# Optimization experiments

Measured on AMD Instinct MI355X. Metric: run time of the kernel, lower is better.

## Reference

```python
import jax, jax.numpy as jnp
import numpy as np

C, CP, H, D, N, B = 128, 16, 8, 16, 2048, 1
INF = 1e8


def _ln(x, w=None, b=None, eps=1e-5):
    mu = jnp.mean(x, axis=-1, keepdims=True)
    var = jnp.var(x, axis=-1, keepdims=True)
    y = (x - mu) * jax.lax.rsqrt(var + eps)
    if w is not None:
        y = y * w
    if b is not None:
        y = y + b
    return y


def _ada_ln(a, s, sln_w, gw, gb, skw):
    # AdaLN: non-affine LN on a, weight-only LN on s, sigmoid gate + skip from s
    a = _ln(a)
    s = _ln(s, sln_w)
    return jax.nn.sigmoid(s @ gw + gb) * a + s @ skw


def _betas(n, n_keys=128, inf=INF):
    # centers at 16 + 32k; query row i belongs to window i//32, keys within +/- n_keys//2 of center
    i = jnp.arange(n)
    c = 16 + 32 * (i // 32)
    j = jnp.arange(n)
    ok = (j[None, :] >= (c - n_keys // 2)[:, None]) & (j[None, :] < (c + n_keys // 2)[:, None])
    return jnp.where(ok, 0.0, -inf).astype(jnp.float32)


def _forward(atom_single, atom_proj, atom_pair, mask,
             a_sln_w, a_gate_w, a_gate_b, a_skip_w,
             wq, bq, wk, wv, wg, bg, wo, bo,
             lnz_w, lnz_b, wz, wog, bog,
             t_sln_w, t_gate_w, t_gate_b, t_skip_w,
             w_sw, w_hid, w_out, t_wog, t_bog):
    bs, n, _ = atom_single.shape
    betas = _betas(n)
    # ---- AttentionPairBias (input_gating=True, residual handled outside) ----
    a = _ada_ln(atom_single, atom_proj, a_sln_w, a_gate_w, a_gate_b, a_skip_w)
    q = (a @ wq + bq).reshape(bs, n, H, D)
    k = (a @ wk).reshape(bs, n, H, D)
    v = (a @ wv).reshape(bs, n, H, D)
    pair_bias = _ln(atom_pair, lnz_w, lnz_b) @ wz            # (bs, n, n, H)
    pair_bias = jnp.transpose(pair_bias, (0, 3, 1, 2)) + betas  # (bs, H, n, n)
    mask_bias = (INF * (mask - 1.0))[:, None, None, :]          # (bs, 1, 1, n)
    logits = jnp.einsum('bqhd,bkhd->bhqk', q, k) / np.float32(np.sqrt(D))
    logits = logits + pair_bias + mask_bias
    probs = jax.nn.softmax(logits, axis=-1)
    o = jnp.einsum('bhqk,bkhd->bqhd', probs, v)
    g = jax.nn.sigmoid(a @ wg + bg).reshape(bs, n, H, D)
    o = (o * g).reshape(bs, n, H * D) @ wo + bo
    o = jax.nn.sigmoid(atom_proj @ wog + bog) * o             # conditioned output gate
    atom_single = atom_single + o
    # ---- ConditionedTransitionBlock (SwiGLU, n=2) ----
    t = _ada_ln(atom_single, atom_proj, t_sln_w, t_gate_w, t_gate_b, t_skip_w)
    hidden = jax.nn.silu(t @ w_sw) * (t @ w_hid)              # (bs, n, 2C)
    t_out = jax.nn.sigmoid(atom_proj @ t_wog + t_bog) * (hidden @ w_out)
    return atom_single + t_out


def setup_inputs() -> dict:
    key = jax.random.key(0)
    ks = iter(jax.random.split(key, 40))
    rn = lambda shape, s=1.0: jax.random.normal(next(ks), shape, jnp.float32) * s
    p = 0.05
    return {
        "atom_single": rn((B, N, C)),
        "atom_proj": rn((B, N, C)),
        "atom_pair": rn((B, N, N, CP)),
        "mask": jnp.ones((B, N), jnp.float32),
        "a_sln_w": jnp.ones((C,), jnp.float32), "a_gate_w": rn((C, C), p), "a_gate_b": jnp.zeros((C,), jnp.float32), "a_skip_w": rn((C, C), p),
        "wq": rn((C, C), p), "bq": jnp.zeros((C,), jnp.float32),
        "wk": rn((C, C), p), "wv": rn((C, C), p),
        "wg": rn((C, C), p), "bg": jnp.ones((C,), jnp.float32),
        "wo": rn((C, C), p), "bo": jnp.zeros((C,), jnp.float32),
        "lnz_w": jnp.ones((CP,), jnp.float32), "lnz_b": jnp.zeros((CP,), jnp.float32), "wz": rn((CP, H), p),
        "wog": rn((C, C), p), "bog": jnp.full((C,), -2.0, jnp.float32),
        "t_sln_w": jnp.ones((C,), jnp.float32), "t_gate_w": rn((C, C), p), "t_gate_b": jnp.zeros((C,), jnp.float32), "t_skip_w": rn((C, C), p),
        "w_sw": rn((C, 2 * C), p), "w_hid": rn((C, 2 * C), p), "w_out": rn((2 * C, C), p),
        "t_wog": rn((C, C), p), "t_bog": jnp.full((C,), -2.0, jnp.float32),
    }


def reference(atom_single, atom_proj, atom_pair, mask,
              a_sln_w, a_gate_w, a_gate_b, a_skip_w,
              wq, bq, wk, wv, wg, bg, wo, bo,
              lnz_w, lnz_b, wz, wog, bog,
              t_sln_w, t_gate_w, t_gate_b, t_skip_w,
              w_sw, w_hid, w_out, t_wog, t_bog):
    out = _forward(atom_single, atom_proj, atom_pair, mask,
                   a_sln_w, a_gate_w, a_gate_b, a_skip_w,
                   wq, bq, wk, wv, wg, bg, wo, bo,
                   lnz_w, lnz_b, wz, wog, bog,
                   t_sln_w, t_gate_w, t_gate_b, t_skip_w,
                   w_sw, w_hid, w_out, t_wog, t_bog)
    return (out, atom_proj, atom_pair)
```

## Files before the change

kernel.cpp:

```cpp
#include <hip/hip_runtime.h>
#include <math.h>

#define NN 2048
#define CC 128
#define HH 8
#define DD 16
#define NKEY 128
#define INFV 1e8f
#define NPR ((long)NN * CC / 4)
#define NCPTOT (NPR + (long)NN * NN * 4)
#define SLOT 2176
#define ANP 36
#define ASLOT 1152

__device__ __forceinline__ float sigm(float x) { return 1.f / (1.f + expf(-x)); }

struct Args {
  const float *atom_single, *atom_proj, *atom_pair, *mask;
  const float *a_sln_w, *a_gate_w, *a_gate_b, *a_skip_w;
  const float *wq, *bq, *wk, *wv, *wg, *bg, *wo, *bo;
  const float *lnz_w, *lnz_b, *wz, *wog, *bog;
  const float *t_sln_w, *t_gate_w, *t_gate_b, *t_skip_w;
  const float *w_sw, *w_hid, *w_out, *t_wog, *t_bog;
  float *out;
  float *s_ln_a, *s_ln_t, *ln_as, *a_mat, *qm, *km, *vm, *gm, *ogm,
        *single2, *t_mat, *hidden, *bias;
  long cut[9];
};

__device__ __forceinline__ void copy_span(const Args& a, int s, long rb, long nb, int tid) {
  long c0 = a.cut[s], c1 = a.cut[s + 1];
  const float4* proj4 = (const float4*)a.atom_proj;
  const float4* pair4 = (const float4*)a.atom_pair;
  float4* dst = (float4*)(a.out + (long)NN * CC);
  long stride = nb * 256;
  long i = c0 + rb * 256 + tid;
  for (; i + 3 * stride < c1; i += 4 * stride) {
    long i1 = i + stride, i2 = i + 2 * stride, i3 = i + 3 * stride;
    float4 x0 = (i  < NPR) ? proj4[i]  : pair4[i  - NPR];
    float4 x1 = (i1 < NPR) ? proj4[i1] : pair4[i1 - NPR];
    float4 x2 = (i2 < NPR) ? proj4[i2] : pair4[i2 - NPR];
    float4 x3 = (i3 < NPR) ? proj4[i3] : pair4[i3 - NPR];
    dst[i] = x0; dst[i1] = x1; dst[i2] = x2; dst[i3] = x3;
  }
  for (; i < c1; i += stride) dst[i] = (i < NPR) ? proj4[i] : pair4[i - NPR];
}

__device__ __forceinline__ void gsingle_pf(float* sm, int tid,
    const float* __restrict__ A1, const float* __restrict__ B1, int lda1, int ldb1, int K1,
    int r0, int c0, float acc1[4][4]) {
  float* buf0 = sm;
  float* buf1 = sm + 2 * SLOT;
  int tr = (tid >> 4) * 4, tc = (tid & 15) * 4;
  int ar = tid >> 5, ak = tid & 31;
  int bk = tid >> 6, bc = tid & 63;
  float pA[2][8], pB[2][8];
  auto LD = [&](int kb, int s) {
#pragma unroll
    for (int j = 0; j < 8; ++j) {
      pA[s][j] = A1[(long)(r0 + ar + 8 * j) * lda1 + kb + ak];
      pB[s][j] = B1[(long)(kb + bk + 4 * j) * ldb1 + c0 + bc];
    }
  };
  auto WR = [&](float* buf, int s) {
    float* B1s_ = buf + SLOT;
#pragma unroll
    for (int j = 0; j < 8; ++j) {
      buf[ak * 68 + ar + 8 * j] = pA[s][j];
      B1s_[(bk + 4 * j) * 68 + bc] = pB[s][j];
    }
  };
  auto CMP = [&](float* cur) {
    float* As_ = cur;
    float* B1s_ = cur + SLOT;
#pragma unroll 4
    for (int k = 0; k < 32; ++k) {
      float4 a1 = *(const float4*)&As_[k * 68 + tr];
      float4 b1 = *(const float4*)&B1s_[k * 68 + tc];
      float a1v[4] = {a1.x, a1.y, a1.z, a1.w};
      float b1v[4] = {b1.x, b1.y, b1.z, b1.w};
#pragma unroll
      for (int i = 0; i < 4; ++i)
#pragma unroll
        for (int j = 0; j < 4; ++j) acc1[i][j] = fmaf(a1v[i], b1v[j], acc1[i][j]);
    }
  };
  int nk = K1 / 32;
  LD(0, 0);
  if (nk > 1) LD(32, 1);
  WR(buf0, 0);
  __syncthreads();
  for (int kt = 0; kt < nk; kt += 2) {
    if (kt + 2 < nk) LD((kt + 2) * 32, 0);
    if (kt + 1 < nk) WR(buf1, 1);
    CMP(buf0);
    __syncthreads();
    if (kt + 1 >= nk) break;
    if (kt + 3 < nk) LD((kt + 3) * 32, 1);
    if (kt + 2 < nk) WR(buf0, 0);
    CMP(buf1);
    __syncthreads();
  }
}

template <bool SHA>
__device__ __forceinline__ void gdual32(float* sm, int tid,
    const float* __restrict__ A1, const float* __restrict__ B1, int lda1, int ldb1, int K1,
    const float* __restrict__ A2, const float* __restrict__ B2, int lda2, int ldb2, int K2,
    int r0, int c0, float acc1[2][4], float acc2[2][4]) {
  const int offB1 = ASLOT;
  const int offA2 = ASLOT + SLOT;
  const int offB2 = SHA ? (ASLOT + SLOT) : (2 * ASLOT + SLOT);
  const int bufsz = SHA ? (ASLOT + 2 * SLOT) : (2 * ASLOT + 2 * SLOT);
  float* buf0 = sm;
  float* buf1 = sm + bufsz;
  int tr2 = (tid >> 4) * 2, tc4 = (tid & 15) * 4;
  int ar = tid & 31, ak4 = (tid >> 5) * 4;
  int bk = tid >> 6, bc = tid & 63;
  float4 vA1[2], vA2[2];
  float pB1[2][8], pB2[2][8];

  auto LD = [&](int kb, int s, bool twof) {
    vA1[s] = *(const float4*)&A1[(long)(r0 + ar) * lda1 + kb + ak4];
#pragma unroll
    for (int j = 0; j < 8; ++j)
      pB1[s][j] = B1[(long)(kb + bk + 4 * j) * ldb1 + c0 + bc];
    if (twof) {
      if constexpr (!SHA) vA2[s] = *(const float4*)&A2[(long)(r0 + ar) * lda2 + kb + ak4];
#pragma unroll
      for (int j = 0; j < 8; ++j)
        pB2[s][j] = B2[(long)(kb + bk + 4 * j) * ldb2 + c0 + bc];
    }
  };
  auto WR = [&](float* buf, int s, bool twof) {
    float* As_ = buf;
    float* B1s_ = buf + offB1;
    As_[(ak4 + 0) * ANP + ar] = vA1[s].x;
    As_[(ak4 + 1) * ANP + ar] = vA1[s].y;
    As_[(ak4 + 2) * ANP + ar] = vA1[s].z;
    As_[(ak4 + 3) * ANP + ar] = vA1[s].w;
#pragma unroll
    for (int j = 0; j < 8; ++j) B1s_[(bk + 4 * j) * 68 + bc] = pB1[s][j];
    if (twof) {
      float* B2s_ = buf + offB2;
      if constexpr (!SHA) {
        float* A2s_ = buf + offA2;
        A2s_[(ak4 + 0) * ANP + ar] = vA2[s].x;
        A2s_[(ak4 + 1) * ANP + ar] = vA2[s].y;
        A2s_[(ak4 + 2) * ANP + ar] = vA2[s].z;
        A2s_[(ak4 + 3) * ANP + ar] = vA2[s].w;
      }
#pragma unroll
      for (int j = 0; j < 8; ++j) B2s_[(bk + 4 * j) * 68 + bc] = pB2[s][j];
    }
  };
  auto CMP = [&](float* cur, bool twoc) {
    float* As_ = cur;
    float* B1s_ = cur + offB1;
    float* A2s_ = cur + offA2;
    float* B2s_ = cur + offB2;
    if (twoc) {
#pragma unroll 4
      for (int k = 0; k < 32; ++k) {
        float2 a1 = *(const float2*)&As_[k * ANP + tr2];
        float4 b1 = *(const float4*)&B1s_[k * 68 + tc4];
        float4 b2 = *(const float4*)&B2s_[k * 68 + tc4];
        float2 a2;
        if constexpr (SHA) a2 = a1; else a2 = *(const float2*)&A2s_[k * ANP + tr2];
        float a1v[2] = {a1.x, a1.y};
        float a2v[2] = {a2.x, a2.y};
        float b1v[4] = {b1.x, b1.y, b1.z, b1.w};
        float b2v[4] = {b2.x, b2.y, b2.z, b2.w};
#pragma unroll
        for (int i = 0; i < 2; ++i)
#pragma unroll
          for (int j = 0; j < 4; ++j) {
            acc1[i][j] = fmaf(a1v[i], b1v[j], acc1[i][j]);
            acc2[i][j] = fmaf(a2v[i], b2v[j], acc2[i][j]);
          }
      }
    } else {
#pragma unroll 4
      for (int k = 0; k < 32; ++k) {
        float2 a1 = *(const float2*)&As_[k * ANP + tr2];
        float4 b1 = *(const float4*)&B1s_[k * 68 + tc4];
        float a1v[2] = {a1.x, a1.y};
        float b1v[4] = {b1.x, b1.y, b1.z, b1.w};
#pragma unroll
        for (int i = 0; i < 2; ++i)
#pragma unroll
          for (int j = 0; j < 4; ++j) acc1[i][j] = fmaf(a1v[i], b1v[j], acc1[i][j]);
      }
    }
  };

  int nk = K1 / 32;
  LD(0, 0, 0 < K2);
  if (nk > 1) LD(32, 1, 32 < K2);
  WR(buf0, 0, 0 < K2);
  __syncthreads();
  for (int kt = 0; kt < nk; kt += 2) {
    if (kt + 2 < nk) LD((kt + 2) * 32, 0, (kt + 2) * 32 < K2);
    if (kt + 1 < nk) WR(buf1, 1, (kt + 1) * 32 < K2);
    CMP(buf0, kt * 32 < K2);
    __syncthreads();
    if (kt + 1 >= nk) break;
    if (kt + 3 < nk) LD((kt + 3) * 32, 1, (kt + 3) * 32 < K2);
    if (kt + 2 < nk) WR(buf0, 0, (kt + 2) * 32 < K2);
    CMP(buf1, (kt + 1) * 32 < K2);
    __syncthreads();
  }
}

__device__ __forceinline__ void bias_stage(const Args& a, long lo, long hi,
                                           int bid, int nb, int tid, float* sm) {
  float* swz = sm;
  float* swn = sm + 128;
  float* sbn = sm + 144;
  if (tid < 128) swz[tid] = a.wz[tid];
  else if (tid < 144) swn[tid - 128] = a.lnz_w[tid - 128];
  else if (tid < 160) sbn[tid - 144] = a.lnz_b[tid - 144];
  __syncthreads();
  for (long e = lo + bid * 256 + tid; e < hi; e += (long)nb * 256) {
    int q = (int)(e >> 7), kk = (int)(e & 127);
    int k = (q >> 5) * 32 - 48 + kk;
    float o[HH];
    if (k >= 0 && k < NN) {
      const float4* p = (const float4*)(a.atom_pair + ((long)q * NN + k) * 16);
      float4 x0 = p[0], x1 = p[1], x2 = p[2], x3 = p[3];
      float x[16] = {x0.x, x0.y, x0.z, x0.w, x1.x, x1.y, x1.z, x1.w,
                     x2.x, x2.y, x2.z, x2.w, x3.x, x3.y, x3.z, x3.w};
      float s = 0.f, ss = 0.f;
#pragma unroll
      for (int c = 0; c < 16; ++c) { s += x[c]; ss += x[c] * x[c]; }
      float mu = s * (1.f / 16.f);
      float r = rsqrtf(ss * (1.f / 16.f) - mu * mu + 1e-5f);
#pragma unroll
      for (int h = 0; h < HH; ++h) o[h] = 0.f;
#pragma unroll
      for (int c = 0; c < 16; ++c) {
        float y = (x[c] - mu) * r * swn[c] + sbn[c];
#pragma unroll
        for (int h = 0; h < HH; ++h) o[h] = fmaf(y, swz[c * HH + h], o[h]);
      }
      float mb = INFV * (a.mask[k] - 1.f);
#pragma unroll
      for (int h = 0; h < HH; ++h) o[h] += mb;
    } else {
#pragma unroll
      for (int h = 0; h < HH; ++h) o[h] = -INFV;
    }
#pragma unroll
    for (int h = 0; h < HH; ++h) a.bias[(long)h * NN * NKEY + e] = o[h];
  }
}

__device__ __forceinline__ void ln1_stage(const Args& a, int lb, int tid) {
  int base = lb * 64;
  int lane = tid & 63;
  for (int r = base + (tid >> 6); r < base + 64; r += 4) {
    {
      float2 v = *(const float2*)(a.atom_single + (long)r * CC + lane * 2);
      float s = v.x + v.y, ss = v.x * v.x + v.y * v.y;
#pragma unroll
      for (int m = 1; m < 64; m <<= 1) { s += __shfl_xor(s, m); ss += __shfl_xor(ss, m); }
      float mu = s * (1.f / CC);
      float rr = rsqrtf(ss * (1.f / CC) - mu * mu + 1e-5f);
      *(float2*)(a.ln_as + (long)r * CC + lane * 2) =
          make_float2((v.x - mu) * rr, (v.y - mu) * rr);
    }
    {
      float2 v = *(const float2*)(a.atom_proj + (long)r * CC + lane * 2);
      float s = v.x + v.y, ss = v.x * v.x + v.y * v.y;
#pragma unroll
      for (int m = 1; m < 64; m <<= 1) { s += __shfl_xor(s, m); ss += __shfl_xor(ss, m); }
      float mu = s * (1.f / CC);
      float rr = rsqrtf(ss * (1.f / CC) - mu * mu + 1e-5f);
      float y0 = (v.x - mu) * rr, y1 = (v.y - mu) * rr;
      float2 wa = *(const float2*)(a.a_sln_w + lane * 2);
      float2 wt = *(const float2*)(a.t_sln_w + lane * 2);
      *(float2*)(a.s_ln_a + (long)r * CC + lane * 2) = make_float2(y0 * wa.x, y1 * wa.y);
      *(float2*)(a.s_ln_t + (long)r * CC + lane * 2) = make_float2(y0 * wt.x, y1 * wt.y);
    }
  }
}

template <bool INLN>
__device__ __forceinline__ void adaln32_stage(const Args& a, const float* A, const float* gw,
                                              const float* gb, const float* skw,
                                              const float* lnm_or_src, float* outp,
                                              int bid, int tid, float* sm, float* sst) {
  int r0 = (bid & 63) * 32, c0 = (bid >> 6) * 64;
  if constexpr (INLN) {
    int row = tid >> 3, cg = (tid & 7) * 16;
    const float* src = lnm_or_src + (long)(r0 + row) * CC + cg;
    float s = 0.f, ss = 0.f;
#pragma unroll
    for (int j = 0; j < 4; ++j) {
      float4 v = *(const float4*)(src + j * 4);
      s += v.x + v.y + v.z + v.w;
      ss += v.x * v.x + v.y * v.y + v.z * v.z + v.w * v.w;
    }
#pragma unroll
    for (int m = 1; m < 8; m <<= 1) { s += __shfl_xor(s, m); ss += __shfl_xor(ss, m); }
    if ((tid & 7) == 0) {
      float mu = s * (1.f / CC);
      sst[2 * row] = mu;
      sst[2 * row + 1] = rsqrtf(ss * (1.f / CC) - mu * mu + 1e-5f);
    }
  }
  float acc1[2][4] = {{0}}, acc2[2][4] = {{0}};
  gdual32<true>(sm, tid, A, gw, 128, 128, 128, A, skw, 128, 128, 128, r0, c0, acc1, acc2);
  int tr2 = (tid >> 4) * 2, tc4 = (tid & 15) * 4;
#pragma unroll
  for (int i = 0; i < 2; ++i) {
    long r = r0 + tr2 + i;
    float lv[4];
    if constexpr (INLN) {
      float mu = sst[2 * (tr2 + i)], rr = sst[2 * (tr2 + i) + 1];
      float4 sv = *(const float4*)(lnm_or_src + r * CC + c0 + tc4);
      lv[0] = (sv.x - mu) * rr; lv[1] = (sv.y - mu) * rr;
      lv[2] = (sv.z - mu) * rr; lv[3] = (sv.w - mu) * rr;
    } else {
      float4 lm = *(const float4*)(lnm_or_src + r * CC + c0 + tc4);
      lv[0] = lm.x; lv[1] = lm.y; lv[2] = lm.z; lv[3] = lm.w;
    }
    float o[4];
#pragma unroll
    for (int j = 0; j < 4; ++j)
      o[j] = sigm(acc1[i][j] + gb[c0 + tc4 + j]) * lv[j] + acc2[i][j];
    *(float4*)(outp + r * CC + c0 + tc4) = make_float4(o[0], o[1], o[2], o[3]);
  }
}

__device__ __forceinline__ void gemm4_stage(const Args& a, int bid, int tid, float* sm) {
  int r0 = (bid & 31) * 64;
  int cg4 = (bid >> 5) * 64;
  int mat = cg4 >> 7;
  int c0 = cg4 & 127;
  const float* B = (mat == 0) ? a.wq : (mat == 1) ? a.wk : (mat == 2) ? a.wv : a.wg;
  float acc[4][4] = {{0}};
  gsingle_pf(sm, tid, a.a_mat, B, 128, 128, 128, r0, c0, acc);
  float* outp = (mat == 0) ? a.qm : (mat == 1) ? a.km : (mat == 2) ? a.vm : a.gm;
  int tr = (tid >> 4) * 4, tc = (tid & 15) * 4;
#pragma unroll
  for (int i = 0; i < 4; ++i) {
    long r = r0 + tr + i;
    float o[4];
#pragma unroll
    for (int j = 0; j < 4; ++j) {
      float x = acc[i][j];
      if (mat == 0) x += a.bq[c0 + tc + j];
      if (mat == 3) x = sigm(x + a.bg[c0 + tc + j]);
      o[j] = x;
    }
    *(float4*)(outp + r * CC + c0 + tc) = make_float4(o[0], o[1], o[2], o[3]);
  }
}

__device__ __forceinline__ void attn_unit(const Args& a, int u, int tid, float* sm) {
  int w = u & 63, h = u >> 6;
  int q0 = w * 32, k0 = w * 32 - 48;
  float* Qs = sm;
  float* Ks = sm + 544;
  float* Vs = sm + 3104;
  float* Ps = sm + 5664;
  for (int i = tid; i < 32 * 16; i += 256) {
    int qi = i >> 4, d = i & 15;
    Qs[qi * 17 + d] = a.qm[(long)(q0 + qi) * CC + h * DD + d];
  }
  for (int i = tid; i < 128 * 16; i += 256) {
    int kk = i >> 4, d = i & 15;
    int k = k0 + kk;
    bool ok = (k >= 0 && k < NN);
    Ks[kk * 20 + d] = ok ? a.km[(long)k * CC + h * DD + d] : 0.f;
    Vs[kk * 20 + d] = ok ? a.vm[(long)k * CC + h * DD + d] : 0.f;
  }
  __syncthreads();
  int qi = tid >> 3, kg = tid & 7;
  const float* brow = a.bias + (long)h * NN * NKEY + (long)(q0 + qi) * NKEY;
  float qreg[16];
#pragma unroll
  for (int d = 0; d < 16; ++d) qreg[d] = Qs[qi * 17 + d];
  float l[16];
#pragma unroll
  for (int j = 0; j < 16; ++j) {
    int kk = kg + 8 * j;
    const float4* kr = (const float4*)&Ks[kk * 20];
    float4 k0v = kr[0], k1v = kr[1], k2v = kr[2], k3v = kr[3];
    float acc = 0.f;
    acc = fmaf(qreg[0], k0v.x, acc);  acc = fmaf(qreg[1], k0v.y, acc);
    acc = fmaf(qreg[2], k0v.z, acc);  acc = fmaf(qreg[3], k0v.w, acc);
    acc = fmaf(qreg[4], k1v.x, acc);  acc = fmaf(qreg[5], k1v.y, acc);
    acc = fmaf(qreg[6], k1v.z, acc);  acc = fmaf(qreg[7], k1v.w, acc);
    acc = fmaf(qreg[8], k2v.x, acc);  acc = fmaf(qreg[9], k2v.y, acc);
    acc = fmaf(qreg[10], k2v.z, acc); acc = fmaf(qreg[11], k2v.w, acc);
    acc = fmaf(qreg[12], k3v.x, acc); acc = fmaf(qreg[13], k3v.y, acc);
    acc = fmaf(qreg[14], k3v.z, acc); acc = fmaf(qreg[15], k3v.w, acc);
    l[j] = acc * 0.25f + brow[kk];
  }
  float m = l[0];
#pragma unroll
  for (int j = 1; j < 16; ++j) m = fmaxf(m, l[j]);
#pragma unroll
  for (int mm = 1; mm < 8; mm <<= 1) m = fmaxf(m, __shfl_xor(m, mm));
  float sum = 0.f;
#pragma unroll
  for (int j = 0; j < 16; ++j) { l[j] = expf(l[j] - m); sum += l[j]; }
#pragma unroll
  for (int mm = 1; mm < 8; mm <<= 1) sum += __shfl_xor(sum, mm);
  float inv = 1.f / sum;
#pragma unroll
  for (int j = 0; j < 16; ++j) Ps[qi * 132 + kg + 8 * j] = l[j] * inv;
  __syncthreads();
  int d0 = tid & 7;
  float o0 = 0.f, o1 = 0.f;
#pragma unroll 8
  for (int kk = 0; kk < 128; ++kk) {
    float p = Ps[qi * 132 + kk];
    o0 = fmaf(p, Vs[kk * 20 + d0], o0);
    o1 = fmaf(p, Vs[kk * 20 + d0 + 8], o1);
  }
  long base = (long)(q0 + qi) * CC + h * DD;
  a.ogm[base + d0] = o0 * a.gm[base + d0];
  a.ogm[base + d0 + 8] = o1 * a.gm[base + d0 + 8];
}

__device__ __forceinline__ void out1_32(const Args& a, int bid, int tid, float* sm) {
  int r0 = (bid & 63) * 32, c0 = (bid >> 6) * 64;
  float accX[2][4] = {{0}}, accW[2][4] = {{0}};
  gdual32<false>(sm, tid, a.ogm, a.wo, 128, 128, 128, a.atom_proj, a.wog, 128, 128, 128,
                 r0, c0, accX, accW);
  int tr2 = (tid >> 4) * 2, tc4 = (tid & 15) * 4;
#pragma unroll
  for (int i = 0; i < 2; ++i) {
    long r = r0 + tr2 + i;
    float4 sv = *(const float4*)(a.atom_single + r * CC + c0 + tc4);
    float s[4] = {sv.x, sv.y, sv.z, sv.w};
    float o[4];
#pragma unroll
    for (int j = 0; j < 4; ++j) {
      int c = c0 + tc4 + j;
      o[j] = s[j] + sigm(accW[i][j] + a.bog[c]) * (accX[i][j] + a.bo[c]);
    }
    *(float4*)(a.single2 + r * CC + c0 + tc4) = make_float4(o[0], o[1], o[2], o[3]);
  }
}

__device__ __forceinline__ void swiglu_32(const Args& a, int bid, int tid, float* sm) {
  int r0 = (bid & 63) * 32, c0 = (bid >> 6) * 64;
  float acc1[2][4] = {{0}}, acc2[2][4] = {{0}};
  gdual32<true>(sm, tid, a.t_mat, a.w_sw, 128, 256, 128, a.t_mat, a.w_hid, 128, 256, 128,
                r0, c0, acc1, acc2);
  int tr2 = (tid >> 4) * 2, tc4 = (tid & 15) * 4;
#pragma unroll
  for (int i = 0; i < 2; ++i) {
    long r = r0 + tr2 + i;
    float o[4];
#pragma unroll
    for (int j = 0; j < 4; ++j) {
      float x = acc1[i][j];
      o[j] = x * sigm(x) * acc2[i][j];
    }
    *(float4*)(a.hidden + r * 256 + c0 + tc4) = make_float4(o[0], o[1], o[2], o[3]);
  }
}

__device__ __forceinline__ void out2_32(const Args& a, int bid, int tid, float* sm) {
  int r0 = (bid & 63) * 32, c0 = (bid >> 6) * 64;
  float accX[2][4] = {{0}}, accW[2][4] = {{0}};
  gdual32<false>(sm, tid, a.hidden, a.w_out, 256, 128, 256, a.atom_proj, a.t_wog, 128, 128, 128,
                 r0, c0, accX, accW);
  int tr2 = (tid >> 4) * 2, tc4 = (tid & 15) * 4;
#pragma unroll
  for (int i = 0; i < 2; ++i) {
    long r = r0 + tr2 + i;
    float4 sv = *(const float4*)(a.single2 + r * CC + c0 + tc4);
    float s[4] = {sv.x, sv.y, sv.z, sv.w};
    float o[4];
#pragma unroll
    for (int j = 0; j < 4; ++j) {
      int c = c0 + tc4 + j;
      o[j] = s[j] + sigm(accW[i][j] + a.t_bog[c]) * accX[i][j];
    }
    *(float4*)(a.out + r * CC + c0 + tc4) = make_float4(o[0], o[1], o[2], o[3]);
  }
}

#define BIAS_TOT ((long)NN * NKEY)
#define BIAS_1 (BIAS_TOT / 3)
#define BIAS_2 (2 * BIAS_TOT / 3)

__global__ __launch_bounds__(256) void k_head(Args a) {
  __shared__ __align__(16) float sm[160];
  int bid = blockIdx.x, tid = threadIdx.x;
  if (bid < 96) bias_stage(a, 0, BIAS_1, bid, 96, tid, sm);
  else if (bid < 128) ln1_stage(a, bid - 96, tid);
  else copy_span(a, 0, bid - 128, gridDim.x - 128, tid);
}

__global__ __launch_bounds__(256) void k_adaln_a(Args a) {
  __shared__ __align__(16) float sm[2 * (ASLOT + 2 * SLOT) + 64];
  int bid = blockIdx.x, tid = threadIdx.x;
  if (bid < 128)
    adaln32_stage<false>(a, a.s_ln_a, a.a_gate_w, a.a_gate_b, a.a_skip_w, a.ln_as, a.a_mat,
                         bid, tid, sm, nullptr);
  else if (bid < 224) bias_stage(a, BIAS_1, BIAS_2, bid - 128, 96, tid, sm);
  else copy_span(a, 1, bid - 224, gridDim.x - 224, tid);
}

__global__ __launch_bounds__(256) void k_qkvg(Args a) {
  __shared__ __align__(16) float sm[2 * 2 * SLOT];
  int bid = blockIdx.x, tid = threadIdx.x;
  if (bid < 256) gemm4_stage(a, bid, tid, sm);
  else if (bid < 352) bias_stage(a, BIAS_2, BIAS_TOT, bid - 256, 96, tid, sm);
  else copy_span(a, 2, bid - 352, gridDim.x - 352, tid);
}

__global__ __launch_bounds__(256) void k_attn(Args a) {
  __shared__ __align__(16) float sm[9888];
  int bid = blockIdx.x, tid = threadIdx.x;
  if (bid < 512) attn_unit(a, bid, tid, sm);
  else copy_span(a, 3, bid - 512, gridDim.x - 512, tid);
}

__global__ __launch_bounds__(256) void k_out1(Args a) {
  __shared__ __align__(16) float sm[2 * (2 * ASLOT + 2 * SLOT)];
  int bid = blockIdx.x, tid = threadIdx.x;
  if (bid < 128) out1_32(a, bid, tid, sm);
  else copy_span(a, 4, bid - 128, gridDim.x - 128, tid);
}

__global__ __launch_bounds__(256) void k_adaln_t(Args a) {
  __shared__ __align__(16) float sm[2 * (ASLOT + 2 * SLOT) + 64];
  int bid = blockIdx.x, tid = threadIdx.x;
  if (bid < 128)
    adaln32_stage<true>(a, a.s_ln_t, a.t_gate_w, a.t_gate_b, a.t_skip_w, a.single2, a.t_mat,
                        bid, tid, sm, sm + 2 * (ASLOT + 2 * SLOT));
  else copy_span(a, 5, bid - 128, gridDim.x - 128, tid);
}

__global__ __launch_bounds__(256) void k_swiglu(Args a) {
  __shared__ __align__(16) float sm[2 * (ASLOT + 2 * SLOT)];
  int bid = blockIdx.x, tid = threadIdx.x;
  if (bid < 256) swiglu_32(a, bid, tid, sm);
  else copy_span(a, 6, bid - 256, gridDim.x - 256, tid);
}

__global__ __launch_bounds__(256) void k_out2(Args a) {
  __shared__ __align__(16) float sm[2 * (2 * ASLOT + 2 * SLOT)];
  int bid = blockIdx.x, tid = threadIdx.x;
  if (bid < 128) out2_32(a, bid, tid, sm);
  else copy_span(a, 7, bid - 128, gridDim.x - 128, tid);
}

extern "C" void kernel_launch(void* const* d_in, const int* in_sizes, int n_in,
                              void* d_out, int out_size, void* d_ws, size_t ws_size,
                              hipStream_t stream) {
  (void)in_sizes; (void)n_in; (void)out_size; (void)ws_size;
  Args a;
  a.atom_single = (const float*)d_in[0];
  a.atom_proj   = (const float*)d_in[1];
  a.atom_pair   = (const float*)d_in[2];
  a.mask        = (const float*)d_in[3];
  a.a_sln_w  = (const float*)d_in[4];
  a.a_gate_w = (const float*)d_in[5];
  a.a_gate_b = (const float*)d_in[6];
  a.a_skip_w = (const float*)d_in[7];
  a.wq = (const float*)d_in[8];  a.bq = (const float*)d_in[9];
  a.wk = (const float*)d_in[10]; a.wv = (const float*)d_in[11];
  a.wg = (const float*)d_in[12]; a.bg = (const float*)d_in[13];
  a.wo = (const float*)d_in[14]; a.bo = (const float*)d_in[15];
  a.lnz_w = (const float*)d_in[16]; a.lnz_b = (const float*)d_in[17];
  a.wz = (const float*)d_in[18];
  a.wog = (const float*)d_in[19]; a.bog = (const float*)d_in[20];
  a.t_sln_w  = (const float*)d_in[21];
  a.t_gate_w = (const float*)d_in[22];
  a.t_gate_b = (const float*)d_in[23];
  a.t_skip_w = (const float*)d_in[24];
  a.w_sw  = (const float*)d_in[25];
  a.w_hid = (const float*)d_in[26];
  a.w_out = (const float*)d_in[27];
  a.t_wog = (const float*)d_in[28];
  a.t_bog = (const float*)d_in[29];
  a.out = (float*)d_out;

  float* ws = (float*)d_ws;
  const long NC = (long)NN * CC;
  a.s_ln_a  = ws + 0 * NC;
  a.s_ln_t  = ws + 1 * NC;
  a.ln_as   = ws + 2 * NC;
  a.a_mat   = ws + 3 * NC;
  a.qm      = ws + 4 * NC;
  a.km      = ws + 5 * NC;
  a.vm      = ws + 6 * NC;
  a.gm      = ws + 7 * NC;
  a.ogm     = ws + 8 * NC;
  a.single2 = ws + 9 * NC;
  a.t_mat   = ws + 11 * NC;
  a.hidden  = ws + 12 * NC;
  a.bias    = ws + 14 * NC;

  const int cum[9] = {0, 8, 15, 26, 40, 46, 52, 58, 64};
  for (int i = 0; i < 9; ++i) a.cut[i] = NCPTOT * (long)cum[i] / 64;

  k_head   <<<2048, 256, 0, stream>>>(a);
  k_adaln_a<<<2048, 256, 0, stream>>>(a);
  k_qkvg   <<<2048, 256, 0, stream>>>(a);
  k_attn   <<<2048, 256, 0, stream>>>(a);
  k_out1   <<<2048, 256, 0, stream>>>(a);
  k_adaln_t<<<2048, 256, 0, stream>>>(a);
  k_swiglu <<<2048, 256, 0, stream>>>(a);
  k_out2   <<<2048, 256, 0, stream>>>(a);
}
```

Before: 159.4 us.

## Fuse input layernorms into AdaLN gate/skip GEMM and drop head kernel

Removes the separate head kernel that layer-normalized atom_single and atom_proj into workspace buffers. The AdaLN-a GEMM now computes per-row LN statistics itself, normalizes A tiles on the fly while loading, and also emits the t-branch scaled LN of atom_proj. The pair-bias work and the passthrough copy are re-split over seven launches instead of eight. This saves one launch and several intermediate global round trips, at the cost of redundant LN statistics per column block and heavier tile loads.

```diff
diff --git a/kernel.cpp b/kernel.cpp
--- a/kernel.cpp
+++ b/kernel.cpp
@@ -23,9 +23,8 @@
   const float *t_sln_w, *t_gate_w, *t_gate_b, *t_skip_w;
   const float *w_sw, *w_hid, *w_out, *t_wog, *t_bog;
   float *out;
-  float *s_ln_a, *s_ln_t, *ln_as, *a_mat, *qm, *km, *vm, *gm, *ogm,
-        *single2, *t_mat, *hidden, *bias;
-  long cut[9];
+  float *s_ln_t, *a_mat, *qm, *km, *vm, *gm, *ogm, *single2, *t_mat, *hidden, *bias;
+  long cut[8];
 };
 
 __device__ __forceinline__ void copy_span(const Args& a, int s, long rb, long nb, int tid) {
@@ -212,6 +211,89 @@
   }
 }
 
+__device__ __forceinline__ void gdual32_ln(float* sm, int tid,
+    const float* __restrict__ proj, const float* __restrict__ w_ln,
+    const float* __restrict__ B1, const float* __restrict__ B2,
+    int r0, int c0, const float* sst, float acc1[2][4], float acc2[2][4]) {
+  const int offB1 = ASLOT;
+  const int offB2 = ASLOT + SLOT;
+  const int bufsz = ASLOT + 2 * SLOT;
+  float* buf0 = sm;
+  float* buf1 = sm + bufsz;
+  int tr2 = (tid >> 4) * 2, tc4 = (tid & 15) * 4;
+  int ar = tid & 31, ak4 = (tid >> 5) * 4;
+  int bk = tid >> 6, bc = tid & 63;
+  float4 vA1[2];
+  float pB1[2][8], pB2[2][8];
+
+  auto LD = [&](int kb, int s) {
+    float4 raw = *(const float4*)&proj[(long)(r0 + ar) * CC + kb + ak4];
+    float4 wv = *(const float4*)&w_ln[kb + ak4];
+    float mu = sst[2 * ar], rs = sst[2 * ar + 1];
+    vA1[s].x = (raw.x - mu) * rs * wv.x;
+    vA1[s].y = (raw.y - mu) * rs * wv.y;
+    vA1[s].z = (raw.z - mu) * rs * wv.z;
+    vA1[s].w = (raw.w - mu) * rs * wv.w;
+#pragma unroll
+    for (int j = 0; j < 8; ++j) {
+      pB1[s][j] = B1[(long)(kb + bk + 4 * j) * CC + c0 + bc];
+      pB2[s][j] = B2[(long)(kb + bk + 4 * j) * CC + c0 + bc];
+    }
+  };
+  auto WR = [&](float* buf, int s) {
+    float* B1s_ = buf + offB1;
+    float* B2s_ = buf + offB2;
+    buf[(ak4 + 0) * ANP + ar] = vA1[s].x;
+    buf[(ak4 + 1) * ANP + ar] = vA1[s].y;
+    buf[(ak4 + 2) * ANP + ar] = vA1[s].z;
+    buf[(ak4 + 3) * ANP + ar] = vA1[s].w;
+#pragma unroll
+    for (int j = 0; j < 8; ++j) {
+      B1s_[(bk + 4 * j) * 68 + bc] = pB1[s][j];
+      B2s_[(bk + 4 * j) * 68 + bc] = pB2[s][j];
+    }
+  };
+  auto CMP = [&](float* cur) {
+    float* As_ = cur;
+    float* B1s_ = cur + offB1;
+    float* B2s_ = cur + offB2;
+#pragma unroll 4
+    for (int k = 0; k < 32; ++k) {
+      float2 a1 = *(const float2*)&As_[k * ANP + tr2];
+      float4 b1 = *(const float4*)&B1s_[k * 68 + tc4];
+      float4 b2 = *(const float4*)&B2s_[k * 68 + tc4];
+      float a1v[2] = {a1.x, a1.y};
+      float b1v[4] = {b1.x, b1.y, b1.z, b1.w};
+      float b2v[4] = {b2.x, b2.y, b2.z, b2.w};
+#pragma unroll
+      for (int i = 0; i < 2; ++i)
+#pragma unroll
+        for (int j = 0; j < 4; ++j) {
+          acc1[i][j] = fmaf(a1v[i], b1v[j], acc1[i][j]);
+          acc2[i][j] = fmaf(a1v[i], b2v[j], acc2[i][j]);
+        }
+    }
+  };
+
+  LD(0, 0);
+  LD(32, 1);
+  WR(buf0, 0);
+  __syncthreads();
+  LD(64, 0);
+  WR(buf1, 1);
+  CMP(buf0);
+  __syncthreads();
+  LD(96, 1);
+  WR(buf0, 0);
+  CMP(buf1);
+  __syncthreads();
+  WR(buf1, 1);
+  CMP(buf0);
+  __syncthreads();
+  CMP(buf1);
+  __syncthreads();
+}
+
 __device__ __forceinline__ void bias_stage(const Args& a, long lo, long hi,
                                            int bid, int nb, int tid, float* sm) {
   float* swz = sm;
@@ -255,33 +337,62 @@
   }
 }
 
-__device__ __forceinline__ void ln1_stage(const Args& a, int lb, int tid) {
-  int base = lb * 64;
-  int lane = tid & 63;
-  for (int r = base + (tid >> 6); r < base + 64; r += 4) {
-    {
-      float2 v = *(const float2*)(a.atom_single + (long)r * CC + lane * 2);
-      float s = v.x + v.y, ss = v.x * v.x + v.y * v.y;
-#pragma unroll
-      for (int m = 1; m < 64; m <<= 1) { s += __shfl_xor(s, m); ss += __shfl_xor(ss, m); }
-      float mu = s * (1.f / CC);
-      float rr = rsqrtf(ss * (1.f / CC) - mu * mu + 1e-5f);
-      *(float2*)(a.ln_as + (long)r * CC + lane * 2) =
-          make_float2((v.x - mu) * rr, (v.y - mu) * rr);
-    }
-    {
-      float2 v = *(const float2*)(a.atom_proj + (long)r * CC + lane * 2);
-      float s = v.x + v.y, ss = v.x * v.x + v.y * v.y;
-#pragma unroll
-      for (int m = 1; m < 64; m <<= 1) { s += __shfl_xor(s, m); ss += __shfl_xor(ss, m); }
-      float mu = s * (1.f / CC);
-      float rr = rsqrtf(ss * (1.f / CC) - mu * mu + 1e-5f);
-      float y0 = (v.x - mu) * rr, y1 = (v.y - mu) * rr;
-      float2 wa = *(const float2*)(a.a_sln_w + lane * 2);
-      float2 wt = *(const float2*)(a.t_sln_w + lane * 2);
-      *(float2*)(a.s_ln_a + (long)r * CC + lane * 2) = make_float2(y0 * wa.x, y1 * wa.y);
-      *(float2*)(a.s_ln_t + (long)r * CC + lane * 2) = make_float2(y0 * wt.x, y1 * wt.y);
-    }
+__device__ __forceinline__ void adaln_a_ln(const Args& a, int bid, int tid,
+                                           float* sm, float* sst) {
+  int r0 = (bid & 63) * 32, c0 = (bid >> 6) * 64;
+  {
+    int row = tid >> 3, cg = (tid & 7) * 16;
+    const float* sp = a.atom_proj + (long)(r0 + row) * CC + cg;
+    const float* ss_ = a.atom_single + (long)(r0 + row) * CC + cg;
+    float s1 = 0.f, q1 = 0.f, s2 = 0.f, q2 = 0.f;
+#pragma unroll
+    for (int j = 0; j < 4; ++j) {
+      float4 v = *(const float4*)(sp + j * 4);
+      s1 += v.x + v.y + v.z + v.w;
+      q1 += v.x * v.x + v.y * v.y + v.z * v.z + v.w * v.w;
+      float4 u = *(const float4*)(ss_ + j * 4);
+      s2 += u.x + u.y + u.z + u.w;
+      q2 += u.x * u.x + u.y * u.y + u.z * u.z + u.w * u.w;
+    }
+#pragma unroll
+    for (int m = 1; m < 8; m <<= 1) {
+      s1 += __shfl_xor(s1, m); q1 += __shfl_xor(q1, m);
+      s2 += __shfl_xor(s2, m); q2 += __shfl_xor(q2, m);
+    }
+    if ((tid & 7) == 0) {
+      float mu1 = s1 * (1.f / CC);
+      sst[2 * row] = mu1;
+      sst[2 * row + 1] = rsqrtf(q1 * (1.f / CC) - mu1 * mu1 + 1e-5f);
+      float mu2 = s2 * (1.f / CC);
+      sst[64 + 2 * row] = mu2;
+      sst[64 + 2 * row + 1] = rsqrtf(q2 * (1.f / CC) - mu2 * mu2 + 1e-5f);
+    }
+  }
+  __syncthreads();
+  float acc1[2][4] = {{0}}, acc2[2][4] = {{0}};
+  gdual32_ln(sm, tid, a.atom_proj, a.a_sln_w, a.a_gate_w, a.a_skip_w,
+             r0, c0, sst, acc1, acc2);
+  int tr2 = (tid >> 4) * 2, tc4 = (tid & 15) * 4;
+#pragma unroll
+  for (int i = 0; i < 2; ++i) {
+    long r = r0 + tr2 + i;
+    float mup = sst[2 * (tr2 + i)], rsp = sst[2 * (tr2 + i) + 1];
+    float mus = sst[64 + 2 * (tr2 + i)], rss = sst[64 + 2 * (tr2 + i) + 1];
+    float4 sv = *(const float4*)(a.atom_single + r * CC + c0 + tc4);
+    float4 pv = *(const float4*)(a.atom_proj + r * CC + c0 + tc4);
+    float4 wt = *(const float4*)(a.t_sln_w + c0 + tc4);
+    float lnm[4] = {(sv.x - mus) * rss, (sv.y - mus) * rss,
+                    (sv.z - mus) * rss, (sv.w - mus) * rss};
+    float lnp[4] = {(pv.x - mup) * rsp, (pv.y - mup) * rsp,
+                    (pv.z - mup) * rsp, (pv.w - mup) * rsp};
+    float wtv[4] = {wt.x, wt.y, wt.z, wt.w};
+    float o[4];
+#pragma unroll
+    for (int j = 0; j < 4; ++j)
+      o[j] = sigm(acc1[i][j] + a.a_gate_b[c0 + tc4 + j]) * lnm[j] + acc2[i][j];
+    *(float4*)(a.a_mat + r * CC + c0 + tc4) = make_float4(o[0], o[1], o[2], o[3]);
+    *(float4*)(a.s_ln_t + r * CC + c0 + tc4) =
+        make_float4(lnp[0] * wtv[0], lnp[1] * wtv[1], lnp[2] * wtv[2], lnp[3] * wtv[3]);
   }
 }
 
@@ -488,47 +599,36 @@
 }
 
 #define BIAS_TOT ((long)NN * NKEY)
-#define BIAS_1 (BIAS_TOT / 3)
-#define BIAS_2 (2 * BIAS_TOT / 3)
-
-__global__ __launch_bounds__(256) void k_head(Args a) {
-  __shared__ __align__(16) float sm[160];
+#define BIAS_H (BIAS_TOT / 2)
+
+__global__ __launch_bounds__(256) void k_adaln_a(Args a) {
+  __shared__ __align__(16) float sm[2 * (ASLOT + 2 * SLOT) + 128];
   int bid = blockIdx.x, tid = threadIdx.x;
-  if (bid < 96) bias_stage(a, 0, BIAS_1, bid, 96, tid, sm);
-  else if (bid < 128) ln1_stage(a, bid - 96, tid);
-  else copy_span(a, 0, bid - 128, gridDim.x - 128, tid);
-}
-
-__global__ __launch_bounds__(256) void k_adaln_a(Args a) {
-  __shared__ __align__(16) float sm[2 * (ASLOT + 2 * SLOT) + 64];
-  int bid = blockIdx.x, tid = threadIdx.x;
-  if (bid < 128)
-    adaln32_stage<false>(a, a.s_ln_a, a.a_gate_w, a.a_gate_b, a.a_skip_w, a.ln_as, a.a_mat,
-                         bid, tid, sm, nullptr);
-  else if (bid < 224) bias_stage(a, BIAS_1, BIAS_2, bid - 128, 96, tid, sm);
-  else copy_span(a, 1, bid - 224, gridDim.x - 224, tid);
+  if (bid < 128) adaln_a_ln(a, bid, tid, sm, sm + 2 * (ASLOT + 2 * SLOT));
+  else if (bid < 256) bias_stage(a, 0, BIAS_H, bid - 128, 128, tid, sm);
+  else copy_span(a, 0, bid - 256, gridDim.x - 256, tid);
 }
 
 __global__ __launch_bounds__(256) void k_qkvg(Args a) {
   __shared__ __align__(16) float sm[2 * 2 * SLOT];
   int bid = blockIdx.x, tid = threadIdx.x;
   if (bid < 256) gemm4_stage(a, bid, tid, sm);
-  else if (bid < 352) bias_stage(a, BIAS_2, BIAS_TOT, bid - 256, 96, tid, sm);
-  else copy_span(a, 2, bid - 352, gridDim.x - 352, tid);
+  else if (bid < 384) bias_stage(a, BIAS_H, BIAS_TOT, bid - 256, 128, tid, sm);
+  else copy_span(a, 1, bid - 384, gridDim.x - 384, tid);
 }
 
 __global__ __launch_bounds__(256) void k_attn(Args a) {
   __shared__ __align__(16) float sm[9888];
   int bid = blockIdx.x, tid = threadIdx.x;
   if (bid < 512) attn_unit(a, bid, tid, sm);
-  else copy_span(a, 3, bid - 512, gridDim.x - 512, tid);
+  else copy_span(a, 2, bid - 512, gridDim.x - 512, tid);
 }
 
 __global__ __launch_bounds__(256) void k_out1(Args a) {
   __shared__ __align__(16) float sm[2 * (2 * ASLOT + 2 * SLOT)];
   int bid = blockIdx.x, tid = threadIdx.x;
   if (bid < 128) out1_32(a, bid, tid, sm);
-  else copy_span(a, 4, bid - 128, gridDim.x - 128, tid);
+  else copy_span(a, 3, bid - 128, gridDim.x - 128, tid);
 }
 
 __global__ __launch_bounds__(256) void k_adaln_t(Args a) {
@@ -537,21 +637,21 @@
   if (bid < 128)
     adaln32_stage<true>(a, a.s_ln_t, a.t_gate_w, a.t_gate_b, a.t_skip_w, a.single2, a.t_mat,
                         bid, tid, sm, sm + 2 * (ASLOT + 2 * SLOT));
-  else copy_span(a, 5, bid - 128, gridDim.x - 128, tid);
+  else copy_span(a, 4, bid - 128, gridDim.x - 128, tid);
 }
 
 __global__ __launch_bounds__(256) void k_swiglu(Args a) {
   __shared__ __align__(16) float sm[2 * (ASLOT + 2 * SLOT)];
   int bid = blockIdx.x, tid = threadIdx.x;
   if (bid < 256) swiglu_32(a, bid, tid, sm);
-  else copy_span(a, 6, bid - 256, gridDim.x - 256, tid);
+  else copy_span(a, 5, bid - 256, gridDim.x - 256, tid);
 }
 
 __global__ __launch_bounds__(256) void k_out2(Args a) {
   __shared__ __align__(16) float sm[2 * (2 * ASLOT + 2 * SLOT)];
   int bid = blockIdx.x, tid = threadIdx.x;
   if (bid < 128) out2_32(a, bid, tid, sm);
-  else copy_span(a, 7, bid - 128, gridDim.x - 128, tid);
+  else copy_span(a, 6, bid - 128, gridDim.x - 128, tid);
 }
 
 extern "C" void kernel_launch(void* const* d_in, const int* in_sizes, int n_in,
@@ -587,24 +687,21 @@
 
   float* ws = (float*)d_ws;
   const long NC = (long)NN * CC;
-  a.s_ln_a  = ws + 0 * NC;
-  a.s_ln_t  = ws + 1 * NC;
-  a.ln_as   = ws + 2 * NC;
-  a.a_mat   = ws + 3 * NC;
-  a.qm      = ws + 4 * NC;
-  a.km      = ws + 5 * NC;
-  a.vm      = ws + 6 * NC;
-  a.gm      = ws + 7 * NC;
-  a.ogm     = ws + 8 * NC;
-  a.single2 = ws + 9 * NC;
-  a.t_mat   = ws + 11 * NC;
-  a.hidden  = ws + 12 * NC;
-  a.bias    = ws + 14 * NC;
-
-  const int cum[9] = {0, 8, 15, 26, 40, 46, 52, 58, 64};
-  for (int i = 0; i < 9; ++i) a.cut[i] = NCPTOT * (long)cum[i] / 64;
-
-  k_head   <<<2048, 256, 0, stream>>>(a);
+  a.s_ln_t  = ws + 0 * NC;
+  a.a_mat   = ws + 1 * NC;
+  a.qm      = ws + 2 * NC;
+  a.km      = ws + 3 * NC;
+  a.vm      = ws + 4 * NC;
+  a.gm      = ws + 5 * NC;
+  a.ogm     = ws + 6 * NC;
+  a.single2 = ws + 7 * NC;
+  a.t_mat   = ws + 8 * NC;
+  a.hidden  = ws + 9 * NC;
+  a.bias    = ws + 11 * NC;
+
+  const int cum[8] = {0, 11, 23, 37, 44, 51, 58, 64};
+  for (int i = 0; i < 8; ++i) a.cut[i] = NCPTOT * (long)cum[i] / 64;
+
   k_adaln_a<<<2048, 256, 0, stream>>>(a);
   k_qkvg   <<<2048, 256, 0, stream>>>(a);
   k_attn   <<<2048, 256, 0, stream>>>(a);
```

New measurement: 145.3 us. 8.8% less time.
